# Kernel optimization log

Hardware: AMD Instinct MI355X
Metric: run time of the kernel (lower is better)

Reference implementation:

```python
import jax, jax.numpy as jnp
import numpy as np

B, S, HID = 2, 4096, 3584
NH, NKV, HD, FD = 16, 8, 256, 64
CHUNK = 64

def _rope_tables(seq_len, dim, base=10000.0):
    inv = 1.0 / (base ** (np.arange(0, dim, 2) / dim))      # [dim/2]
    f = np.outer(np.arange(seq_len), inv)                   # [S, dim/2]
    return jnp.asarray(np.cos(f), jnp.float32), jnp.asarray(np.sin(f), jnp.float32)

def setup_inputs() -> dict:
    key = jax.random.key(0)
    ks = jax.random.split(key, 8)
    def w(k, shape, fan):
        return jax.random.normal(k, shape, jnp.float32) * (fan ** -0.5)
    cos, sin = _rope_tables(S, HD)
    return dict(
        hidden_states=jax.random.normal(ks[0], (B, S, HID), jnp.float32),
        cos=cos, sin=sin,
        Wq=w(ks[1], (HID, NH * HD), HID),
        Wk=w(ks[2], (HID, NKV * HD), HID),
        Wv=w(ks[3], (HID, NKV * HD), HID),
        Wo=w(ks[4], (NH * HD, HID), NH * HD),
        fmq=w(ks[5], (NH, HD, FD), HD),
        fmk=w(ks[6], (NH, HD, FD), HD),
    )

def apply_rope(x, cos, sin):
    # Gemma split-half rotary. x: [B,S,h,D]; cos/sin: [S,D/2]
    d2 = x.shape[-1] // 2
    x1, x2 = x[..., :d2], x[..., d2:]
    c = cos[None, :, None, :]
    s = sin[None, :, None, :]
    return jnp.concatenate([x1 * c - x2 * s, x1 * s + x2 * c], axis=-1)

def feature_map(x, w):
    # Hedgehog: per-head linear then cat(softmax(z), softmax(-z)).
    # x: [B,h,S,D], w: [h,D,F] -> [B,h,S,2F]
    z = jnp.einsum('bhsd,hdf->bhsf', x, w)
    return jnp.concatenate([jax.nn.softmax(z, axis=-1), jax.nn.softmax(-z, axis=-1)], axis=-1)

def chunk_linear_attn(q, k, v, chunk=CHUNK):
    # q,k: [B,H,T,dk]; v: [B,H,T,dv]; T divisible by chunk (S=4096, chunk=64)
    b, h, T, dk = q.shape
    dv = v.shape[-1]
    n = T // chunk
    q = q.reshape(b, h, n, chunk, dk) * (dk ** -0.5)
    k = k.reshape(b, h, n, chunk, dk)
    v = v.reshape(b, h, n, chunk, dv)
    kv = jnp.einsum('bhncd,bhnce->bhnde', k, v)          # per-chunk K^T V: [b,h,n,dk,dv]
    kv = jnp.cumsum(kv, axis=2)
    kv = jnp.concatenate([jnp.zeros_like(kv[:, :, :1]), kv[:, :, :-1]], axis=2)  # exclusive
    inter = jnp.einsum('bhncd,bhnde->bhnce', q, kv)
    scores = jnp.einsum('bhncd,bhnkd->bhnck', q, k)
    causal = jnp.tril(jnp.ones((chunk, chunk), dtype=bool))
    scores = jnp.where(causal, scores, jnp.zeros((), scores.dtype))
    intra = jnp.einsum('bhnck,bhnke->bhnce', scores, v)
    return (inter + intra).reshape(b, h, T, dv)

def reference(hidden_states, cos, sin, Wq, Wk, Wv, Wo, fmq, fmk):
    b, s, _ = hidden_states.shape
    q = (hidden_states @ Wq).reshape(b, s, NH, HD)
    k = (hidden_states @ Wk).reshape(b, s, NKV, HD)
    v = (hidden_states @ Wv).reshape(b, s, NKV, HD)
    q = apply_rope(q, cos, sin)
    k = apply_rope(k, cos, sin)
    g = NH // NKV
    k = jnp.repeat(k, g, axis=2)   # GQA expansion
    v = jnp.repeat(v, g, axis=2)
    q = q.transpose(0, 2, 1, 3)    # [B,H,S,D]
    k = k.transpose(0, 2, 1, 3)
    v = v.transpose(0, 2, 1, 3)
    q = feature_map(q, fmq)        # [B,H,S,2F]
    k = feature_map(k, fmk)
    o = chunk_linear_attn(q, k, v)                      # [B,H,S,HD]
    o = o.transpose(0, 2, 1, 3).reshape(b, s, NH * HD)
    return o @ Wo
```

## Files before the change

kernel.cpp:

```cpp
#include <hip/hip_runtime.h>

typedef float  f32x4  __attribute__((ext_vector_type(4)));
typedef __bf16 bf16x4 __attribute__((ext_vector_type(4)));
typedef __bf16 bf16x8 __attribute__((ext_vector_type(8)));

#define MFMA16(a,b,c) __builtin_amdgcn_mfma_f32_16x16x32_bf16((a),(b),(c),0,0,0)

__device__ __forceinline__ void async_copy16(void* lds, const void* gmem) {
  __builtin_amdgcn_global_load_lds(
      (const __attribute__((address_space(1))) void*)gmem,
      (__attribute__((address_space(3))) void*)lds, 16, 0, 0);
}

template<int N> __device__ __forceinline__ void vmcnt_gate() {
  if constexpr (N == 8) asm volatile("s_waitcnt vmcnt(8)" ::: "memory");
  else if constexpr (N == 6) asm volatile("s_waitcnt vmcnt(6)" ::: "memory");
  else if constexpr (N == 4) asm volatile("s_waitcnt vmcnt(4)" ::: "memory");
  else if constexpr (N == 2) asm volatile("s_waitcnt vmcnt(2)" ::: "memory");
  else if constexpr (N == 0) asm volatile("s_waitcnt vmcnt(0)" ::: "memory");
  __builtin_amdgcn_sched_barrier(0);
}

#define LGKM(N) do { __builtin_amdgcn_sched_barrier(0); \
                     asm volatile("s_waitcnt lgkmcnt(" #N ")" ::: "memory"); \
                     __builtin_amdgcn_sched_barrier(0); } while (0)

#define BARRIER do { __builtin_amdgcn_sched_barrier(0); \
                     __builtin_amdgcn_s_barrier(); \
                     __builtin_amdgcn_sched_barrier(0); } while (0)

__global__ __launch_bounds__(256) void convert_kernel(const float* __restrict__ in,
                                                      __bf16* __restrict__ out, size_t n4) {
  size_t i = (size_t)blockIdx.x * 256 + threadIdx.x;
  if (i >= n4) return;
  f32x4 v = *(const f32x4*)(in + i * 4);
  bf16x4 o;
  #pragma unroll
  for (int j = 0; j < 4; ++j) o[j] = (__bf16)v[j];
  *(bf16x4*)(out + i * 4) = o;
}

__global__ __launch_bounds__(256) void transpose_kernel(const float* __restrict__ in,
                                                        __bf16* __restrict__ out, int R, int C) {
  __shared__ float tile[32][33];
  int bx = blockIdx.x, by = blockIdx.y;
  int tx = threadIdx.x & 31, ty0 = threadIdx.x >> 5;
  #pragma unroll
  for (int i = 0; i < 4; ++i) {
    int r = by * 32 + ty0 + i * 8;
    tile[ty0 + i * 8][tx] = in[(size_t)r * C + bx * 32 + tx];
  }
  __syncthreads();
  #pragma unroll
  for (int i = 0; i < 4; ++i) {
    int c = bx * 32 + ty0 + i * 8;
    out[(size_t)c * R + by * 32 + tx] = (__bf16)tile[tx][ty0 + i * 8];
  }
}


template<bool REMAP>
__device__ __forceinline__ void stage_q(__bf16* region, int qrow, const __bf16* src,
                                        int K, int w, int l) {
  int s = qrow + w * 8 + (l >> 3);
  int gr = REMAP ? (((s >> 5) << 4) | (s & 15) | (((s >> 4) & 1) << 7)) : s;
  async_copy16(region + (size_t)(qrow + w * 8) * 64,
               src + (size_t)gr * K + (((l & 7) ^ (s & 7)) << 3));
}

template<bool LATE, bool EARLY, bool NEXT, int G2, int G3, bool BMAP>
__device__ __forceinline__ void tile_body(__bf16* smem,
                                          const __bf16* Apan, const __bf16* Bpan,
                                          int K, int tau, int wm, int wn,
                                          int lo, int hi, int w, int l,
                                          bf16x8 (&aA)[4], bf16x8 (&aB)[4],
                                          bf16x8 (&bA)[4], bf16x8 (&bB)[4],
                                          f32x4 (&acc)[8][4]) {
  const int buf = tau & 1;
  __bf16* Ab = smem + buf * 32768;
  __bf16* Bb = Ab + 16384;
  __bf16* An = smem + (buf ^ 1) * 32768;
  __bf16* Bn = An + 16384;

  #pragma unroll
  for (int t = 0; t < 4; ++t) {
    int ra = wm * 128 + 64 + t * 16 + lo;
    aB[t] = *(const bf16x8*)(Ab + (size_t)ra * 64 + ((hi ^ (ra & 7)) << 3));
  }
  if constexpr (LATE) {
    const __bf16* Ap1 = Apan + (size_t)(tau + 1) * 64;
    stage_q<false>(An, 64,  Ap1, K, w, l);
    stage_q<false>(An, 192, Ap1, K, w, l);
  }
  LGKM(4);
  __builtin_amdgcn_s_setprio(1);
  #pragma unroll
  for (int mt = 0; mt < 4; ++mt)
    #pragma unroll
    for (int nt = 0; nt < 4; ++nt)
      acc[mt][nt] = MFMA16(aA[mt], bA[nt], acc[mt][nt]);
  __builtin_amdgcn_s_setprio(0);
  BARRIER;

  #pragma unroll
  for (int t = 0; t < 4; ++t) {
    int ra = wm * 128 + t * 16 + lo;
    aA[t] = *(const bf16x8*)(Ab + (size_t)ra * 64 + (((4 + hi) ^ (ra & 7)) << 3));
  }
  #pragma unroll
  for (int t = 0; t < 4; ++t) {
    int rb = wn * 64 + t * 16 + lo;
    bB[t] = *(const bf16x8*)(Bb + (size_t)rb * 64 + (((4 + hi) ^ (rb & 7)) << 3));
  }
  LGKM(8);
  __builtin_amdgcn_s_setprio(1);
  #pragma unroll
  for (int mt = 0; mt < 4; ++mt)
    #pragma unroll
    for (int nt = 0; nt < 4; ++nt)
      acc[4 + mt][nt] = MFMA16(aB[mt], bA[nt], acc[4 + mt][nt]);
  __builtin_amdgcn_s_setprio(0);
  BARRIER;

  #pragma unroll
  for (int t = 0; t < 4; ++t) {
    int ra = wm * 128 + 64 + t * 16 + lo;
    aB[t] = *(const bf16x8*)(Ab + (size_t)ra * 64 + (((4 + hi) ^ (ra & 7)) << 3));
  }
  LGKM(4);
  __builtin_amdgcn_s_setprio(1);
  #pragma unroll
  for (int mt = 0; mt < 4; ++mt)
    #pragma unroll
    for (int nt = 0; nt < 4; ++nt)
      acc[mt][nt] = MFMA16(aA[mt], bB[nt], acc[mt][nt]);
  __builtin_amdgcn_s_setprio(0);
  if constexpr (G2 >= 0) vmcnt_gate<G2>();
  BARRIER;

  if constexpr (NEXT) {
    #pragma unroll
    for (int t = 0; t < 4; ++t) {
      int ra = wm * 128 + t * 16 + lo;
      aA[t] = *(const bf16x8*)(An + (size_t)ra * 64 + ((hi ^ (ra & 7)) << 3));
    }
    #pragma unroll
    for (int t = 0; t < 4; ++t) {
      int rb = wn * 64 + t * 16 + lo;
      bA[t] = *(const bf16x8*)(Bn + (size_t)rb * 64 + ((hi ^ (rb & 7)) << 3));
    }
  }
  if constexpr (EARLY) {
    const __bf16* Ap2 = Apan + (size_t)(tau + 2) * 64;
    const __bf16* Bp2 = Bpan + (size_t)(tau + 2) * 64;
    stage_q<false>(Ab, 0,   Ap2, K, w, l);
    stage_q<false>(Ab, 128, Ap2, K, w, l);
    stage_q<BMAP>(Bb, 0,   Bp2, K, w, l);
    stage_q<BMAP>(Bb, 64,  Bp2, K, w, l);
    stage_q<BMAP>(Bb, 128, Bp2, K, w, l);
    stage_q<BMAP>(Bb, 192, Bp2, K, w, l);
  }
  if constexpr (NEXT) LGKM(8); else LGKM(0);
  __builtin_amdgcn_s_setprio(1);
  #pragma unroll
  for (int mt = 0; mt < 4; ++mt)
    #pragma unroll
    for (int nt = 0; nt < 4; ++nt)
      acc[4 + mt][nt] = MFMA16(aB[mt], bB[nt], acc[4 + mt][nt]);
  __builtin_amdgcn_s_setprio(0);
  if constexpr (G3 >= 0) vmcnt_gate<G3>();
  BARRIER;
}

template <typename CT, int MODE>
__global__ __launch_bounds__(512, 2) void gemm256_kernel(const __bf16* __restrict__ A,
                                                         const __bf16* __restrict__ Bt,
                                                         CT* __restrict__ C, int M, int N, int K,
                                                         const float* __restrict__ cosT,
                                                         const float* __restrict__ sinT,
                                                         int Hh) {
  extern __shared__ __bf16 smem[];
  constexpr bool BMAP = (MODE == 1);

  const int gx = gridDim.x;
  const int nwg = gx * gridDim.y;
  const int wg = blockIdx.y * gx + blockIdx.x;
  const int qq = nwg >> 3;
  const int id2 = (wg & 7) * qq + (wg >> 3);
  const int m0 = (id2 / gx) * 256, n0 = (id2 % gx) * 256;

  const int tid = threadIdx.x;
  const int l = tid & 63, w = tid >> 6;
  const int lo = l & 15, hi = l >> 4;
  const int wm = w >> 2, wn = w & 3;

  const __bf16* Apan = A + (size_t)m0 * K;
  const __bf16* Bpan = Bt + (size_t)n0 * K;

  f32x4 acc[8][4] = {};
  bf16x8 aA[4], aB[4], bA[4], bB[4];

  stage_q<false>(smem,          0,   Apan, K, w, l);
  stage_q<false>(smem,          128, Apan, K, w, l);
  stage_q<BMAP>(smem + 16384,  0,   Bpan, K, w, l);
  stage_q<BMAP>(smem + 16384,  64,  Bpan, K, w, l);
  stage_q<BMAP>(smem + 16384,  128, Bpan, K, w, l);
  stage_q<BMAP>(smem + 16384,  192, Bpan, K, w, l);
  stage_q<false>(smem,          64,  Apan, K, w, l);
  stage_q<false>(smem,          192, Apan, K, w, l);
  stage_q<false>(smem + 32768,  0,   Apan + 64, K, w, l);
  stage_q<false>(smem + 32768,  128, Apan + 64, K, w, l);
  stage_q<BMAP>(smem + 49152,  0,   Bpan + 64, K, w, l);
  stage_q<BMAP>(smem + 49152,  64,  Bpan + 64, K, w, l);
  stage_q<BMAP>(smem + 49152,  128, Bpan + 64, K, w, l);
  stage_q<BMAP>(smem + 49152,  192, Bpan + 64, K, w, l);
  stage_q<false>(smem + 32768,  64,  Apan + 64, K, w, l);
  stage_q<false>(smem + 32768,  192, Apan + 64, K, w, l);
  vmcnt_gate<8>();
  BARRIER;

  #pragma unroll
  for (int t = 0; t < 4; ++t) {
    int ra = wm * 128 + t * 16 + lo;
    aA[t] = *(const bf16x8*)(smem + (size_t)ra * 64 + ((hi ^ (ra & 7)) << 3));
  }
  #pragma unroll
  for (int t = 0; t < 4; ++t) {
    int rb = wn * 64 + t * 16 + lo;
    bA[t] = *(const bf16x8*)(smem + 16384 + (size_t)rb * 64 + ((hi ^ (rb & 7)) << 3));
  }

  const int T = K >> 6;
  tile_body<false, true,  true,  2,  6, BMAP>(smem, Apan, Bpan, K, 0,     wm, wn, lo, hi, w, l, aA, aB, bA, bB, acc);
  for (int tau = 1; tau < T - 2; ++tau)
    tile_body<true, true,  true,  2,  6, BMAP>(smem, Apan, Bpan, K, tau,   wm, wn, lo, hi, w, l, aA, aB, bA, bB, acc);
  tile_body<true,  false, true,  2,  0, BMAP>(smem, Apan, Bpan, K, T - 2, wm, wn, lo, hi, w, l, aA, aB, bA, bB, acc);
  tile_body<false, false, false, -1, -1, BMAP>(smem, Apan, Bpan, K, T - 1, wm, wn, lo, hi, w, l, aA, aB, bA, bB, acc);

  if constexpr (MODE == 0) {
    #pragma unroll
    for (int mt = 0; mt < 8; ++mt)
      #pragma unroll
      for (int nt = 0; nt < 4; ++nt) {
        int col = n0 + wn * 64 + nt * 16 + lo;
        #pragma unroll
        for (int r = 0; r < 4; ++r) {
          int row = m0 + wm * 128 + mt * 16 + 4 * hi + r;
          C[(size_t)row * N + col] = (CT)acc[mt][nt][r];
        }
      }
  } else if constexpr (MODE == 2) {
    const int kv = n0 >> 8;
    #pragma unroll
    for (int mt = 0; mt < 8; ++mt)
      #pragma unroll
      for (int nt = 0; nt < 4; ++nt) {
        int col = wn * 64 + nt * 16 + lo;
        #pragma unroll
        for (int r = 0; r < 4; ++r) {
          int row = m0 + wm * 128 + mt * 16 + 4 * hi + r;
          int bb = row >> 12, sdx = row & 4095;
          C[(((size_t)(bb * Hh + kv)) * 4096 + sdx) * 256 + col] = (CT)acc[mt][nt][r];
        }
      }
  } else {
    const int hq = n0 >> 8;
    #pragma unroll
    for (int mt = 0; mt < 8; ++mt)
      #pragma unroll
      for (int ntp = 0; ntp < 4; ntp += 2) {
        int d = (2 * wn + (ntp >> 1)) * 16 + lo;
        #pragma unroll
        for (int r = 0; r < 4; ++r) {
          int row = m0 + wm * 128 + mt * 16 + 4 * hi + r;
          int bb = row >> 12, sdx = row & 4095;
          float cc = cosT[(size_t)sdx * 128 + d];
          float ss = sinT[(size_t)sdx * 128 + d];
          float x1 = acc[mt][ntp][r], x2 = acc[mt][ntp + 1][r];
          size_t base = (((size_t)(bb * Hh + hq)) * 4096 + sdx) * 256;
          C[base + d]       = (CT)(x1 * cc - x2 * ss);
          C[base + d + 128] = (CT)(x1 * ss + x2 * cc);
        }
      }
  }
}

__global__ __launch_bounds__(256) void fm_kernel(const __bf16* __restrict__ rope,
                                                 const float* __restrict__ fm,
                                                 __bf16* __restrict__ out, int srcH, float scale) {
  __shared__ __bf16 fmT[64][256];
  int bh = blockIdx.y;
  int h = bh & 15, b = bh >> 4;
  int s0 = blockIdx.x * 128;
  int tid = threadIdx.x, lane = tid & 63, wid = tid >> 6, hi = lane >> 4, lo = lane & 15;

  const float* fmh = fm + (size_t)h * 256 * 64;
  for (int i = tid; i < 256 * 64; i += 256) {
    int d = i >> 6, f = i & 63;
    fmT[f][(((d >> 3) ^ (f & 7)) << 3) | (d & 7)] = (__bf16)fmh[i];
  }
  __syncthreads();

  int srch = (srcH == 16) ? h : (h >> 1);
  const __bf16* abase = rope + ((size_t)(b * srcH + srch) * 4096 + s0 + 32 * wid) * 256;
  f32x4 acc[2][4] = {};
  for (int kk = 0; kk < 256; kk += 32) {
    bf16x8 a[2], bf[4];
    #pragma unroll
    for (int mt = 0; mt < 2; ++mt)
      a[mt] = *(const bf16x8*)(abase + (size_t)(16 * mt + lo) * 256 + kk + 8 * hi);
    const int G = (kk >> 3) + hi;
    #pragma unroll
    for (int nt = 0; nt < 4; ++nt) {
      int f = 16 * nt + lo;
      bf[nt] = *(const bf16x8*)&fmT[f][(G ^ (f & 7)) << 3];
    }
    #pragma unroll
    for (int mt = 0; mt < 2; ++mt)
      #pragma unroll
      for (int nt = 0; nt < 4; ++nt)
        acc[mt][nt] = MFMA16(a[mt], bf[nt], acc[mt][nt]);
  }

  size_t obase = ((size_t)(b * 16 + h) * 4096 + s0 + 32 * wid);
  #pragma unroll
  for (int mt = 0; mt < 2; ++mt) {
    #pragma unroll
    for (int r = 0; r < 4; ++r) {
      float z0 = acc[mt][0][r], z1 = acc[mt][1][r], z2 = acc[mt][2][r], z3 = acc[mt][3][r];
      float mx = fmaxf(fmaxf(z0, z1), fmaxf(z2, z3));
      float mn = fminf(fminf(z0, z1), fminf(z2, z3));
      #pragma unroll
      for (int off = 1; off < 16; off <<= 1) {
        mx = fmaxf(mx, __shfl_xor(mx, off));
        mn = fminf(mn, __shfl_xor(mn, off));
      }
      float ep0 = __expf(z0 - mx), ep1 = __expf(z1 - mx), ep2 = __expf(z2 - mx), ep3 = __expf(z3 - mx);
      float en0 = __expf(mn - z0), en1 = __expf(mn - z1), en2 = __expf(mn - z2), en3 = __expf(mn - z3);
      float sp = ep0 + ep1 + ep2 + ep3, sn = en0 + en1 + en2 + en3;
      #pragma unroll
      for (int off = 1; off < 16; off <<= 1) {
        sp += __shfl_xor(sp, off);
        sn += __shfl_xor(sn, off);
      }
      float rp = scale / sp, rn = scale / sn;
      int row = 16 * mt + 4 * hi + r;
      __bf16* op = out + (obase + row) * 128;
      op[0  + lo] = (__bf16)(ep0 * rp);  op[16 + lo] = (__bf16)(ep1 * rp);
      op[32 + lo] = (__bf16)(ep2 * rp);  op[48 + lo] = (__bf16)(ep3 * rp);
      op[64 + lo] = (__bf16)(en0 * rn);  op[80 + lo] = (__bf16)(en1 * rn);
      op[96 + lo] = (__bf16)(en2 * rn);  op[112 + lo] = (__bf16)(en3 * rn);
    }
  }
}

__global__ __launch_bounds__(256) void attn_kernel(const __bf16* __restrict__ qf,
                                                   const __bf16* __restrict__ kf,
                                                   const __bf16* __restrict__ vp,
                                                   __bf16* __restrict__ o) {
  __shared__ __bf16 k_s[64][128];
  __shared__ __bf16 vT_s[32][64];
  __shared__ __bf16 sc_s[64][64];
  __shared__ __bf16 STb[32][128];

  int bid = blockIdx.x;
  int dvb = bid & 7, h = (bid >> 3) & 15, b = bid >> 7;
  int dv0 = dvb * 32;
  int tid = threadIdx.x, lane = tid & 63, wid = tid >> 6, hi = lane >> 4, lo = lane & 15;

  const __bf16* qh = qf + ((size_t)(b * 16 + h)) * 4096 * 128;
  const __bf16* kh = kf + ((size_t)(b * 16 + h)) * 4096 * 128;
  const __bf16* vh = vp + ((size_t)(b * 8 + (h >> 1))) * 4096 * 256 + dv0;
  __bf16* oh = o + ((size_t)b * 4096) * 4096 + h * 256 + dv0;

  {
    unsigned int* z = (unsigned int*)&STb[0][0];
    for (int i = tid; i < 2048; i += 256) z[i] = 0u;
  }
  f32x4 st[2][2] = {};

  for (int n = 0; n < 64; ++n) {
    int s0 = n * 64;
    #pragma unroll
    for (int i = 0; i < 4; ++i) {
      int rb = (wid * 4 + i) * 4;
      int r = rb + (lane >> 4);
      int Glog = (lane & 15) ^ (r & 7);
      async_copy16(&k_s[rb][0], kh + (size_t)(s0 + r) * 128 + Glog * 8);
    }
    {
      int c = tid >> 2, d8 = (tid & 3) * 8;
      bf16x8 vv = *(const bf16x8*)(vh + (size_t)(s0 + c) * 256 + d8);
      #pragma unroll
      for (int j = 0; j < 8; ++j) {
        int dv = d8 + j;
        vT_s[dv][(((c >> 3) ^ (dv & 7)) << 3) | (c & 7)] = vv[j];
      }
    }
    __syncthreads();

    bf16x8 aq[4];
    #pragma unroll
    for (int kq = 0; kq < 4; ++kq)
      aq[kq] = *(const bf16x8*)(qh + (size_t)(s0 + 16 * wid + lo) * 128 + 32 * kq + 8 * hi);

    f32x4 acc_o[2] = {}, sacc[4] = {};
    #pragma unroll
    for (int nt = 0; nt < 2; ++nt)
      #pragma unroll
      for (int kq = 0; kq < 4; ++kq) {
        int rr = 16 * nt + lo, G = 4 * kq + hi;
        bf16x8 bf = *(const bf16x8*)&STb[rr][(G ^ (rr & 7)) << 3];
        acc_o[nt] = MFMA16(aq[kq], bf, acc_o[nt]);
      }
    #pragma unroll
    for (int nt = 0; nt < 4; ++nt)
      #pragma unroll
      for (int kq = 0; kq < 4; ++kq) {
        int rr = 16 * nt + lo, G = 4 * kq + hi;
        bf16x8 bf = *(const bf16x8*)&k_s[rr][(G ^ (rr & 7)) << 3];
        sacc[nt] = MFMA16(aq[kq], bf, sacc[nt]);
      }
    #pragma unroll
    for (int nt = 0; nt < 4; ++nt)
      #pragma unroll
      for (int r = 0; r < 4; ++r) {
        int c = 16 * wid + 4 * hi + r;
        int cp = 16 * nt + lo;
        float v = (cp <= c) ? sacc[nt][r] : 0.0f;
        sc_s[c][(((cp >> 3) ^ (c & 7)) << 3) | (cp & 7)] = (__bf16)v;
      }
    asm volatile("" ::: "memory");
    #pragma unroll
    for (int nt = 0; nt < 2; ++nt)
      #pragma unroll
      for (int kq = 0; kq < 2; ++kq) {
        int rA = 16 * wid + lo, GA = 4 * kq + hi;
        bf16x8 af = *(const bf16x8*)&sc_s[rA][(GA ^ (rA & 7)) << 3];
        int rB = 16 * nt + lo;
        bf16x8 bf = *(const bf16x8*)&vT_s[rB][(GA ^ (rB & 7)) << 3];
        acc_o[nt] = MFMA16(af, bf, acc_o[nt]);
      }
    #pragma unroll
    for (int nt = 0; nt < 2; ++nt)
      #pragma unroll
      for (int r = 0; r < 4; ++r) {
        int c = 16 * wid + 4 * hi + r;
        oh[(size_t)(s0 + c) * 4096 + 16 * nt + lo] = (__bf16)acc_o[nt][r];
      }
    __syncthreads();

    bf16x8 bu[2][2];
    #pragma unroll
    for (int q = 0; q < 2; ++q) {
      int dk = 16 * (2 * wid + q) + lo;
      #pragma unroll
      for (int kq = 0; kq < 2; ++kq) {
        bf16x8 tmp;
        #pragma unroll
        for (int j = 0; j < 8; ++j) {
          int c = 32 * kq + 8 * hi + j;
          tmp[j] = k_s[c][(((dk >> 3) ^ (c & 7)) << 3) | (dk & 7)];
        }
        bu[q][kq] = tmp;
      }
    }
    #pragma unroll
    for (int mt = 0; mt < 2; ++mt)
      #pragma unroll
      for (int kq = 0; kq < 2; ++kq) {
        int rA = 16 * mt + lo, GA = 4 * kq + hi;
        bf16x8 av = *(const bf16x8*)&vT_s[rA][(GA ^ (rA & 7)) << 3];
        #pragma unroll
        for (int q = 0; q < 2; ++q)
          st[mt][q] = MFMA16(av, bu[q][kq], st[mt][q]);
      }
    #pragma unroll
    for (int mt = 0; mt < 2; ++mt)
      #pragma unroll
      for (int q = 0; q < 2; ++q) {
        int dk = 16 * (2 * wid + q) + lo;
        #pragma unroll
        for (int r = 0; r < 4; ++r) {
          int dvr = 16 * mt + 4 * hi + r;
          STb[dvr][(((dk >> 3) ^ (dvr & 7)) << 3) | (dk & 7)] = (__bf16)st[mt][q][r];
        }
      }
    __syncthreads();
  }
}

extern "C" void kernel_launch(void* const* d_in, const int* in_sizes, int n_in,
                              void* d_out, int out_size, void* d_ws, size_t ws_size,
                              hipStream_t stream) {
  (void)in_sizes; (void)n_in; (void)out_size; (void)ws_size;
  const float* hs   = (const float*)d_in[0];
  const float* cosT = (const float*)d_in[1];
  const float* sinT = (const float*)d_in[2];
  const float* Wq   = (const float*)d_in[3];
  const float* Wk   = (const float*)d_in[4];
  const float* Wv   = (const float*)d_in[5];
  const float* Wo   = (const float*)d_in[6];
  const float* fmq  = (const float*)d_in[7];
  const float* fmk  = (const float*)d_in[8];
  float* out = (float*)d_out;
  char* ws = (char*)d_ws;

  hipFuncSetAttribute((const void*)gemm256_kernel<float, 0>,
                      hipFuncAttributeMaxDynamicSharedMemorySize, 131072);
  hipFuncSetAttribute((const void*)gemm256_kernel<__bf16, 1>,
                      hipFuncAttributeMaxDynamicSharedMemorySize, 131072);
  hipFuncSetAttribute((const void*)gemm256_kernel<__bf16, 2>,
                      hipFuncAttributeMaxDynamicSharedMemorySize, 131072);

  const size_t MB = 1024ull * 1024ull;
  __bf16* Xb   = (__bf16*)(ws + 0);
  __bf16* qfb  = (__bf16*)(ws + 0);
  __bf16* kfb  = (__bf16*)(ws + 34 * MB);
  __bf16* Wqt  = (__bf16*)(ws + 70 * MB);
  __bf16* ob   = (__bf16*)(ws + 70 * MB);
  __bf16* Wkt  = (__bf16*)(ws + 104 * MB);
  __bf16* Wvt  = (__bf16*)(ws + 119 * MB);
  __bf16* Wot  = (__bf16*)(ws + 140 * MB);
  __bf16* ropq = (__bf16*)(ws + 170 * MB);
  __bf16* ropk = (__bf16*)(ws + 238 * MB);
  __bf16* vpb  = (__bf16*)(ws + 272 * MB);

  convert_kernel<<<28672, 256, 0, stream>>>(hs, Xb, (size_t)8192 * 3584 / 4);
  transpose_kernel<<<dim3(128, 112), 256, 0, stream>>>(Wq, Wqt, 3584, 4096);
  transpose_kernel<<<dim3(64, 112),  256, 0, stream>>>(Wk, Wkt, 3584, 2048);
  transpose_kernel<<<dim3(64, 112),  256, 0, stream>>>(Wv, Wvt, 3584, 2048);
  transpose_kernel<<<dim3(112, 128), 256, 0, stream>>>(Wo, Wot, 4096, 3584);

  gemm256_kernel<__bf16, 1><<<dim3(16, 32), 512, 131072, stream>>>(
      Xb, Wqt, ropq, 8192, 4096, 3584, cosT, sinT, 16);
  gemm256_kernel<__bf16, 1><<<dim3(8, 32),  512, 131072, stream>>>(
      Xb, Wkt, ropk, 8192, 2048, 3584, cosT, sinT, 8);
  gemm256_kernel<__bf16, 2><<<dim3(8, 32),  512, 131072, stream>>>(
      Xb, Wvt, vpb, 8192, 2048, 3584, nullptr, nullptr, 8);

  fm_kernel<<<dim3(32, 32), 256, 0, stream>>>(ropq, fmq, qfb, 16, 0.08838834764831845f);
  fm_kernel<<<dim3(32, 32), 256, 0, stream>>>(ropk, fmk, kfb, 8, 1.0f);

  attn_kernel<<<256, 256, 0, stream>>>(qfb, kfb, vpb, ob);

  gemm256_kernel<float, 0><<<dim3(14, 32), 512, 131072, stream>>>(
      ob, Wot, out, 8192, 3584, 4096, nullptr, nullptr, 0);
}
```

Before: 957.7 us.

## Shrink GEMM tiles from 256x256 to 128x128 with 4-wave workgroups

Replaces the 256x256 tile, 512-thread GEMM with a 128x128 tile, 256-thread variant that uses half the LDS. The goal is more workgroups and better tail/CU balance on the projection GEMMs (e.g. the 14x32 grid for the output projection). The RoPE column remap and head indexing are adjusted with a block offset so a 128-wide tile lands inside a 256-wide head. The cost is lower arithmetic intensity per tile, so there is more global/L2 traffic and per-K-step sync overhead.

```diff
diff --git a/kernel.cpp b/kernel.cpp
--- a/kernel.cpp
+++ b/kernel.cpp
@@ -61,9 +61,10 @@
 
 template<bool REMAP>
 __device__ __forceinline__ void stage_q(__bf16* region, int qrow, const __bf16* src,
-                                        int K, int w, int l) {
+                                        int K, int boff, int w, int l) {
   int s = qrow + w * 8 + (l >> 3);
-  int gr = REMAP ? (((s >> 5) << 4) | (s & 15) | (((s >> 4) & 1) << 7)) : s;
+  int g = boff + s;
+  int gr = REMAP ? (((g >> 5) << 4) | (g & 15) | (((g >> 4) & 1) << 7)) : s;
   async_copy16(region + (size_t)(qrow + w * 8) * 64,
                src + (size_t)gr * K + (((l & 7) ^ (s & 7)) << 3));
 }
@@ -71,31 +72,31 @@
 template<bool LATE, bool EARLY, bool NEXT, int G2, int G3, bool BMAP>
 __device__ __forceinline__ void tile_body(__bf16* smem,
                                           const __bf16* Apan, const __bf16* Bpan,
-                                          int K, int tau, int wm, int wn,
+                                          int K, int boff, int tau, int wm, int wn,
                                           int lo, int hi, int w, int l,
-                                          bf16x8 (&aA)[4], bf16x8 (&aB)[4],
+                                          bf16x8 (&aA)[2], bf16x8 (&aB)[2],
                                           bf16x8 (&bA)[4], bf16x8 (&bB)[4],
-                                          f32x4 (&acc)[8][4]) {
+                                          f32x4 (&acc)[4][4]) {
   const int buf = tau & 1;
-  __bf16* Ab = smem + buf * 32768;
-  __bf16* Bb = Ab + 16384;
-  __bf16* An = smem + (buf ^ 1) * 32768;
-  __bf16* Bn = An + 16384;
-
-  #pragma unroll
-  for (int t = 0; t < 4; ++t) {
-    int ra = wm * 128 + 64 + t * 16 + lo;
+  __bf16* Ab = smem + buf * 16384;
+  __bf16* Bb = Ab + 8192;
+  __bf16* An = smem + (buf ^ 1) * 16384;
+  __bf16* Bn = An + 8192;
+
+  #pragma unroll
+  for (int t = 0; t < 2; ++t) {
+    int ra = wm * 64 + 32 + t * 16 + lo;
     aB[t] = *(const bf16x8*)(Ab + (size_t)ra * 64 + ((hi ^ (ra & 7)) << 3));
   }
   if constexpr (LATE) {
     const __bf16* Ap1 = Apan + (size_t)(tau + 1) * 64;
-    stage_q<false>(An, 64,  Ap1, K, w, l);
-    stage_q<false>(An, 192, Ap1, K, w, l);
-  }
-  LGKM(4);
+    stage_q<false>(An, 32, Ap1, K, 0, w, l);
+    stage_q<false>(An, 96, Ap1, K, 0, w, l);
+  }
+  LGKM(2);
   __builtin_amdgcn_s_setprio(1);
   #pragma unroll
-  for (int mt = 0; mt < 4; ++mt)
+  for (int mt = 0; mt < 2; ++mt)
     #pragma unroll
     for (int nt = 0; nt < 4; ++nt)
       acc[mt][nt] = MFMA16(aA[mt], bA[nt], acc[mt][nt]);
@@ -103,8 +104,8 @@
   BARRIER;
 
   #pragma unroll
-  for (int t = 0; t < 4; ++t) {
-    int ra = wm * 128 + t * 16 + lo;
+  for (int t = 0; t < 2; ++t) {
+    int ra = wm * 64 + t * 16 + lo;
     aA[t] = *(const bf16x8*)(Ab + (size_t)ra * 64 + (((4 + hi) ^ (ra & 7)) << 3));
   }
   #pragma unroll
@@ -112,25 +113,25 @@
     int rb = wn * 64 + t * 16 + lo;
     bB[t] = *(const bf16x8*)(Bb + (size_t)rb * 64 + (((4 + hi) ^ (rb & 7)) << 3));
   }
-  LGKM(8);
+  LGKM(6);
   __builtin_amdgcn_s_setprio(1);
   #pragma unroll
-  for (int mt = 0; mt < 4; ++mt)
+  for (int mt = 0; mt < 2; ++mt)
     #pragma unroll
     for (int nt = 0; nt < 4; ++nt)
-      acc[4 + mt][nt] = MFMA16(aB[mt], bA[nt], acc[4 + mt][nt]);
+      acc[2 + mt][nt] = MFMA16(aB[mt], bA[nt], acc[2 + mt][nt]);
   __builtin_amdgcn_s_setprio(0);
   BARRIER;
 
   #pragma unroll
-  for (int t = 0; t < 4; ++t) {
-    int ra = wm * 128 + 64 + t * 16 + lo;
+  for (int t = 0; t < 2; ++t) {
+    int ra = wm * 64 + 32 + t * 16 + lo;
     aB[t] = *(const bf16x8*)(Ab + (size_t)ra * 64 + (((4 + hi) ^ (ra & 7)) << 3));
   }
-  LGKM(4);
+  LGKM(2);
   __builtin_amdgcn_s_setprio(1);
   #pragma unroll
-  for (int mt = 0; mt < 4; ++mt)
+  for (int mt = 0; mt < 2; ++mt)
     #pragma unroll
     for (int nt = 0; nt < 4; ++nt)
       acc[mt][nt] = MFMA16(aA[mt], bB[nt], acc[mt][nt]);
@@ -140,8 +141,8 @@
 
   if constexpr (NEXT) {
     #pragma unroll
-    for (int t = 0; t < 4; ++t) {
-      int ra = wm * 128 + t * 16 + lo;
+    for (int t = 0; t < 2; ++t) {
+      int ra = wm * 64 + t * 16 + lo;
       aA[t] = *(const bf16x8*)(An + (size_t)ra * 64 + ((hi ^ (ra & 7)) << 3));
     }
     #pragma unroll
@@ -153,27 +154,27 @@
   if constexpr (EARLY) {
     const __bf16* Ap2 = Apan + (size_t)(tau + 2) * 64;
     const __bf16* Bp2 = Bpan + (size_t)(tau + 2) * 64;
-    stage_q<false>(Ab, 0,   Ap2, K, w, l);
-    stage_q<false>(Ab, 128, Ap2, K, w, l);
-    stage_q<BMAP>(Bb, 0,   Bp2, K, w, l);
-    stage_q<BMAP>(Bb, 64,  Bp2, K, w, l);
-    stage_q<BMAP>(Bb, 128, Bp2, K, w, l);
-    stage_q<BMAP>(Bb, 192, Bp2, K, w, l);
-  }
-  if constexpr (NEXT) LGKM(8); else LGKM(0);
+    stage_q<false>(Ab, 0,  Ap2, K, 0, w, l);
+    stage_q<false>(Ab, 64, Ap2, K, 0, w, l);
+    stage_q<BMAP>(Bb, 0,  Bp2, K, boff, w, l);
+    stage_q<BMAP>(Bb, 32, Bp2, K, boff, w, l);
+    stage_q<BMAP>(Bb, 64, Bp2, K, boff, w, l);
+    stage_q<BMAP>(Bb, 96, Bp2, K, boff, w, l);
+  }
+  if constexpr (NEXT) LGKM(6); else LGKM(0);
   __builtin_amdgcn_s_setprio(1);
   #pragma unroll
-  for (int mt = 0; mt < 4; ++mt)
+  for (int mt = 0; mt < 2; ++mt)
     #pragma unroll
     for (int nt = 0; nt < 4; ++nt)
-      acc[4 + mt][nt] = MFMA16(aB[mt], bB[nt], acc[4 + mt][nt]);
+      acc[2 + mt][nt] = MFMA16(aB[mt], bB[nt], acc[2 + mt][nt]);
   __builtin_amdgcn_s_setprio(0);
   if constexpr (G3 >= 0) vmcnt_gate<G3>();
   BARRIER;
 }
 
 template <typename CT, int MODE>
-__global__ __launch_bounds__(512, 2) void gemm256_kernel(const __bf16* __restrict__ A,
+__global__ __launch_bounds__(256, 2) void gemm128_kernel(const __bf16* __restrict__ A,
                                                          const __bf16* __restrict__ Bt,
                                                          CT* __restrict__ C, int M, int N, int K,
                                                          const float* __restrict__ cosT,
@@ -187,78 +188,81 @@
   const int wg = blockIdx.y * gx + blockIdx.x;
   const int qq = nwg >> 3;
   const int id2 = (wg & 7) * qq + (wg >> 3);
-  const int m0 = (id2 / gx) * 256, n0 = (id2 % gx) * 256;
+  const int m0 = (id2 / gx) * 128, n0 = (id2 % gx) * 128;
 
   const int tid = threadIdx.x;
   const int l = tid & 63, w = tid >> 6;
   const int lo = l & 15, hi = l >> 4;
-  const int wm = w >> 2, wn = w & 3;
+  const int wm = w >> 1, wn = w & 1;
 
   const __bf16* Apan = A + (size_t)m0 * K;
-  const __bf16* Bpan = Bt + (size_t)n0 * K;
-
-  f32x4 acc[8][4] = {};
-  bf16x8 aA[4], aB[4], bA[4], bB[4];
-
-  stage_q<false>(smem,          0,   Apan, K, w, l);
-  stage_q<false>(smem,          128, Apan, K, w, l);
-  stage_q<BMAP>(smem + 16384,  0,   Bpan, K, w, l);
-  stage_q<BMAP>(smem + 16384,  64,  Bpan, K, w, l);
-  stage_q<BMAP>(smem + 16384,  128, Bpan, K, w, l);
-  stage_q<BMAP>(smem + 16384,  192, Bpan, K, w, l);
-  stage_q<false>(smem,          64,  Apan, K, w, l);
-  stage_q<false>(smem,          192, Apan, K, w, l);
-  stage_q<false>(smem + 32768,  0,   Apan + 64, K, w, l);
-  stage_q<false>(smem + 32768,  128, Apan + 64, K, w, l);
-  stage_q<BMAP>(smem + 49152,  0,   Bpan + 64, K, w, l);
-  stage_q<BMAP>(smem + 49152,  64,  Bpan + 64, K, w, l);
-  stage_q<BMAP>(smem + 49152,  128, Bpan + 64, K, w, l);
-  stage_q<BMAP>(smem + 49152,  192, Bpan + 64, K, w, l);
-  stage_q<false>(smem + 32768,  64,  Apan + 64, K, w, l);
-  stage_q<false>(smem + 32768,  192, Apan + 64, K, w, l);
+  const int nb = BMAP ? (n0 & ~255) : n0;
+  const int boff = BMAP ? (n0 & 255) : 0;
+  const __bf16* Bpan = Bt + (size_t)nb * K;
+
+  f32x4 acc[4][4] = {};
+  bf16x8 aA[2], aB[2], bA[4], bB[4];
+
+  stage_q<false>(smem,         0,  Apan, K, 0, w, l);
+  stage_q<false>(smem,         64, Apan, K, 0, w, l);
+  stage_q<BMAP>(smem + 8192,   0,  Bpan, K, boff, w, l);
+  stage_q<BMAP>(smem + 8192,   32, Bpan, K, boff, w, l);
+  stage_q<BMAP>(smem + 8192,   64, Bpan, K, boff, w, l);
+  stage_q<BMAP>(smem + 8192,   96, Bpan, K, boff, w, l);
+  stage_q<false>(smem,         32, Apan, K, 0, w, l);
+  stage_q<false>(smem,         96, Apan, K, 0, w, l);
+  stage_q<false>(smem + 16384, 0,  Apan + 64, K, 0, w, l);
+  stage_q<false>(smem + 16384, 64, Apan + 64, K, 0, w, l);
+  stage_q<BMAP>(smem + 24576,  0,  Bpan + 64, K, boff, w, l);
+  stage_q<BMAP>(smem + 24576,  32, Bpan + 64, K, boff, w, l);
+  stage_q<BMAP>(smem + 24576,  64, Bpan + 64, K, boff, w, l);
+  stage_q<BMAP>(smem + 24576,  96, Bpan + 64, K, boff, w, l);
+  stage_q<false>(smem + 16384, 32, Apan + 64, K, 0, w, l);
+  stage_q<false>(smem + 16384, 96, Apan + 64, K, 0, w, l);
   vmcnt_gate<8>();
   BARRIER;
 
   #pragma unroll
-  for (int t = 0; t < 4; ++t) {
-    int ra = wm * 128 + t * 16 + lo;
+  for (int t = 0; t < 2; ++t) {
+    int ra = wm * 64 + t * 16 + lo;
     aA[t] = *(const bf16x8*)(smem + (size_t)ra * 64 + ((hi ^ (ra & 7)) << 3));
   }
   #pragma unroll
   for (int t = 0; t < 4; ++t) {
     int rb = wn * 64 + t * 16 + lo;
-    bA[t] = *(const bf16x8*)(smem + 16384 + (size_t)rb * 64 + ((hi ^ (rb & 7)) << 3));
+    bA[t] = *(const bf16x8*)(smem + 8192 + (size_t)rb * 64 + ((hi ^ (rb & 7)) << 3));
   }
 
   const int T = K >> 6;
-  tile_body<false, true,  true,  2,  6, BMAP>(smem, Apan, Bpan, K, 0,     wm, wn, lo, hi, w, l, aA, aB, bA, bB, acc);
+  tile_body<false, true,  true,  2,  6, BMAP>(smem, Apan, Bpan, K, boff, 0,     wm, wn, lo, hi, w, l, aA, aB, bA, bB, acc);
   for (int tau = 1; tau < T - 2; ++tau)
-    tile_body<true, true,  true,  2,  6, BMAP>(smem, Apan, Bpan, K, tau,   wm, wn, lo, hi, w, l, aA, aB, bA, bB, acc);
-  tile_body<true,  false, true,  2,  0, BMAP>(smem, Apan, Bpan, K, T - 2, wm, wn, lo, hi, w, l, aA, aB, bA, bB, acc);
-  tile_body<false, false, false, -1, -1, BMAP>(smem, Apan, Bpan, K, T - 1, wm, wn, lo, hi, w, l, aA, aB, bA, bB, acc);
+    tile_body<true, true,  true,  2,  6, BMAP>(smem, Apan, Bpan, K, boff, tau,   wm, wn, lo, hi, w, l, aA, aB, bA, bB, acc);
+  tile_body<true,  false, true,  2,  0, BMAP>(smem, Apan, Bpan, K, boff, T - 2, wm, wn, lo, hi, w, l, aA, aB, bA, bB, acc);
+  tile_body<false, false, false, -1, -1, BMAP>(smem, Apan, Bpan, K, boff, T - 1, wm, wn, lo, hi, w, l, aA, aB, bA, bB, acc);
 
   if constexpr (MODE == 0) {
     #pragma unroll
-    for (int mt = 0; mt < 8; ++mt)
+    for (int mt = 0; mt < 4; ++mt)
       #pragma unroll
       for (int nt = 0; nt < 4; ++nt) {
         int col = n0 + wn * 64 + nt * 16 + lo;
         #pragma unroll
         for (int r = 0; r < 4; ++r) {
-          int row = m0 + wm * 128 + mt * 16 + 4 * hi + r;
+          int row = m0 + wm * 64 + mt * 16 + 4 * hi + r;
           C[(size_t)row * N + col] = (CT)acc[mt][nt][r];
         }
       }
   } else if constexpr (MODE == 2) {
     const int kv = n0 >> 8;
-    #pragma unroll
-    for (int mt = 0; mt < 8; ++mt)
+    const int colb = n0 & 255;
+    #pragma unroll
+    for (int mt = 0; mt < 4; ++mt)
       #pragma unroll
       for (int nt = 0; nt < 4; ++nt) {
-        int col = wn * 64 + nt * 16 + lo;
+        int col = colb + wn * 64 + nt * 16 + lo;
         #pragma unroll
         for (int r = 0; r < 4; ++r) {
-          int row = m0 + wm * 128 + mt * 16 + 4 * hi + r;
+          int row = m0 + wm * 64 + mt * 16 + 4 * hi + r;
           int bb = row >> 12, sdx = row & 4095;
           C[(((size_t)(bb * Hh + kv)) * 4096 + sdx) * 256 + col] = (CT)acc[mt][nt][r];
         }
@@ -266,13 +270,13 @@
   } else {
     const int hq = n0 >> 8;
     #pragma unroll
-    for (int mt = 0; mt < 8; ++mt)
+    for (int mt = 0; mt < 4; ++mt)
       #pragma unroll
       for (int ntp = 0; ntp < 4; ntp += 2) {
-        int d = (2 * wn + (ntp >> 1)) * 16 + lo;
+        int d = ((boff >> 5) + 2 * wn + (ntp >> 1)) * 16 + lo;
         #pragma unroll
         for (int r = 0; r < 4; ++r) {
-          int row = m0 + wm * 128 + mt * 16 + 4 * hi + r;
+          int row = m0 + wm * 64 + mt * 16 + 4 * hi + r;
           int bb = row >> 12, sdx = row & 4095;
           float cc = cosT[(size_t)sdx * 128 + d];
           float ss = sinT[(size_t)sdx * 128 + d];
@@ -506,12 +510,12 @@
   float* out = (float*)d_out;
   char* ws = (char*)d_ws;
 
-  hipFuncSetAttribute((const void*)gemm256_kernel<float, 0>,
-                      hipFuncAttributeMaxDynamicSharedMemorySize, 131072);
-  hipFuncSetAttribute((const void*)gemm256_kernel<__bf16, 1>,
-                      hipFuncAttributeMaxDynamicSharedMemorySize, 131072);
-  hipFuncSetAttribute((const void*)gemm256_kernel<__bf16, 2>,
-                      hipFuncAttributeMaxDynamicSharedMemorySize, 131072);
+  hipFuncSetAttribute((const void*)gemm128_kernel<float, 0>,
+                      hipFuncAttributeMaxDynamicSharedMemorySize, 65536);
+  hipFuncSetAttribute((const void*)gemm128_kernel<__bf16, 1>,
+                      hipFuncAttributeMaxDynamicSharedMemorySize, 65536);
+  hipFuncSetAttribute((const void*)gemm128_kernel<__bf16, 2>,
+                      hipFuncAttributeMaxDynamicSharedMemorySize, 65536);
 
   const size_t MB = 1024ull * 1024ull;
   __bf16* Xb   = (__bf16*)(ws + 0);
@@ -532,11 +536,11 @@
   transpose_kernel<<<dim3(64, 112),  256, 0, stream>>>(Wv, Wvt, 3584, 2048);
   transpose_kernel<<<dim3(112, 128), 256, 0, stream>>>(Wo, Wot, 4096, 3584);
 
-  gemm256_kernel<__bf16, 1><<<dim3(16, 32), 512, 131072, stream>>>(
+  gemm128_kernel<__bf16, 1><<<dim3(32, 64), 256, 65536, stream>>>(
       Xb, Wqt, ropq, 8192, 4096, 3584, cosT, sinT, 16);
-  gemm256_kernel<__bf16, 1><<<dim3(8, 32),  512, 131072, stream>>>(
+  gemm128_kernel<__bf16, 1><<<dim3(16, 64), 256, 65536, stream>>>(
       Xb, Wkt, ropk, 8192, 2048, 3584, cosT, sinT, 8);
-  gemm256_kernel<__bf16, 2><<<dim3(8, 32),  512, 131072, stream>>>(
+  gemm128_kernel<__bf16, 2><<<dim3(16, 64), 256, 65536, stream>>>(
       Xb, Wvt, vpb, 8192, 2048, 3584, nullptr, nullptr, 8);
 
   fm_kernel<<<dim3(32, 32), 256, 0, stream>>>(ropq, fmq, qfb, 16, 0.08838834764831845f);
@@ -544,6 +548,6 @@
 
   attn_kernel<<<256, 256, 0, stream>>>(qfb, kfb, vpb, ob);
 
-  gemm256_kernel<float, 0><<<dim3(14, 32), 512, 131072, stream>>>(
+  gemm128_kernel<float, 0><<<dim3(28, 64), 256, 65536, stream>>>(
       ob, Wot, out, 8192, 3584, 4096, nullptr, nullptr, 0);
 }
```

Result: slower. 1.102 ms (+15.1%).
